# Kernel optimization log

Hardware: AMD Instinct MI355X
Metric: run time of the kernel (lower is better)

## Reference

```python
import jax, jax.numpy as jnp
import numpy as np

TEMPERATURE = 8.0  # sqrt(d_k) with d_k = 64


def setup_inputs() -> dict:
    key = jax.random.key(0)
    ks = jax.random.split(key, 5)
    shape = (64, 1024, 64)  # [B*H, N, d_k]
    return {
        "q": jax.random.normal(ks[0], shape, dtype=jnp.float32),
        "k": jax.random.normal(ks[1], shape, dtype=jnp.float32),
        "v": jax.random.normal(ks[2], shape, dtype=jnp.float32),
        "q_sem": jax.random.normal(ks[3], shape, dtype=jnp.float32),
        "k_sem": jax.random.normal(ks[4], shape, dtype=jnp.float32),
    }


def reference(q, k, v, q_sem, k_sem):
    # Semantic fusion branch (q_sem is not None): scores are recomputed
    # with the fused queries/keys. (The original also computes an unused
    # softmax over the pre-fusion scores and an unused attn_sem bmm --
    # dead code with no effect on outputs, so omitted.)
    qf = q + q_sem
    kf = k + k_sem
    attn_score = jnp.einsum("bnd,bmd->bnm", qf, kf) / TEMPERATURE  # [BH, N, N]
    attn = jax.nn.softmax(attn_score, axis=2)
    # dropout in eval mode == identity
    output = jnp.einsum("bnm,bmd->bnd", attn, v)  # [BH, N, d_k]
    return (output, attn, attn_score)
```

## Files before the change

kernel.cpp:

```cpp
#include <hip/hip_runtime.h>
#include <math.h>


#define BH 64
#define N 1024
#define D 64
#define TM 32
#define TK 128
#define NC (N / TK)
#define PSTR 1032
#define VSTR 136

typedef float    f32x4 __attribute__((ext_vector_type(4)));
typedef _Float16 half8 __attribute__((ext_vector_type(8)));
typedef _Float16 half4 __attribute__((ext_vector_type(4)));

__global__ __launch_bounds__(512, 2) void attn_mfma_kernel(
    const float* __restrict__ q, const float* __restrict__ k,
    const float* __restrict__ v, const float* __restrict__ qs,
    const float* __restrict__ ks,
    float* __restrict__ out_o, float* __restrict__ out_a,
    float* __restrict__ out_s)
{
    __shared__ __align__(16) _Float16 Pl[TM][PSTR];
    __shared__ __align__(16) _Float16 VT[2][D][VSTR];
    __shared__ float rsum[TM];

    const int t  = threadIdx.x;
    const int w  = t >> 6;
    const int l  = t & 63;
    const int lr = l & 15;
    const int lg = l >> 4;

    const int wg = blockIdx.x;
    const int b  = ((wg >> 8) << 3) | (wg & 7);
    const int q0 = ((wg >> 3) & 31) * TM;

    const size_t inb = (size_t)b * (N * D);
    const size_t sb  = (size_t)b * N * N + (size_t)q0 * N;

    if (t < TM) rsum[t] = 0.0f;

    half8 qa[2][2];
    {
        const float* qp  = q  + inb + (size_t)(q0 + lr) * D + lg * 8;
        const float* qsp = qs + inb + (size_t)(q0 + lr) * D + lg * 8;
#pragma unroll
        for (int mi = 0; mi < 2; ++mi) {
#pragma unroll
            for (int kst = 0; kst < 2; ++kst) {
                const float* p1 = qp  + mi * 16 * D + kst * 32;
                const float* p2 = qsp + mi * 16 * D + kst * 32;
                f32x4 a0 = *(const f32x4*)p1;
                f32x4 a1 = *(const f32x4*)(p1 + 4);
                f32x4 c0 = *(const f32x4*)p2;
                f32x4 c1 = *(const f32x4*)(p2 + 4);
                half8 h;
#pragma unroll
                for (int i = 0; i < 4; ++i) {
                    h[i]     = (_Float16)(a0[i] + c0[i]);
                    h[i + 4] = (_Float16)(a1[i] + c1[i]);
                }
                qa[mi][kst] = h;
            }
        }
    }
    __syncthreads();

    float rs[8];
#pragma unroll
    for (int i = 0; i < 8; ++i) rs[i] = 0.0f;

    const float* kp0 = k  + inb + (size_t)(w * 16 + lr) * D + lg * 8;
    const float* sp0 = ks + inb + (size_t)(w * 16 + lr) * D + lg * 8;

    f32x4 bufA[8], bufB[8];

    auto LD = [&](f32x4* bf, int kc) {
        const float* kp = kp0 + (size_t)kc * (TK * D);
        const float* sp = sp0 + (size_t)kc * (TK * D);
#pragma unroll
        for (int kst = 0; kst < 2; ++kst) {
            bf[kst * 2 + 0] = *(const f32x4*)(kp + kst * 32);
            bf[kst * 2 + 1] = *(const f32x4*)(kp + kst * 32 + 4);
            bf[kst * 2 + 4] = *(const f32x4*)(sp + kst * 32);
            bf[kst * 2 + 5] = *(const f32x4*)(sp + kst * 32 + 4);
        }
    };

    auto CHUNK = [&](const f32x4* bf, int kc) {
        half8 kb[2];
#pragma unroll
        for (int kst = 0; kst < 2; ++kst) {
            half8 h;
#pragma unroll
            for (int i = 0; i < 4; ++i) {
                h[i]     = (_Float16)(bf[kst * 2 + 0][i] + bf[kst * 2 + 4][i]);
                h[i + 4] = (_Float16)(bf[kst * 2 + 1][i] + bf[kst * 2 + 5][i]);
            }
            kb[kst] = h;
        }
        f32x4 ac0 = {0.f, 0.f, 0.f, 0.f}, ac1 = {0.f, 0.f, 0.f, 0.f};
        ac0 = __builtin_amdgcn_mfma_f32_16x16x32_f16(qa[0][0], kb[0], ac0, 0, 0, 0);
        ac0 = __builtin_amdgcn_mfma_f32_16x16x32_f16(qa[0][1], kb[1], ac0, 0, 0, 0);
        ac1 = __builtin_amdgcn_mfma_f32_16x16x32_f16(qa[1][0], kb[0], ac1, 0, 0, 0);
        ac1 = __builtin_amdgcn_mfma_f32_16x16x32_f16(qa[1][1], kb[1], ac1, 0, 0, 0);

        const int col = kc * TK + w * 16 + lr;
#pragma unroll
        for (int mi = 0; mi < 2; ++mi) {
            const f32x4 av = mi ? ac1 : ac0;
#pragma unroll
            for (int r = 0; r < 4; ++r) {
                const int row = mi * 16 + lg * 4 + r;
                const float sv = av[r] * 0.125f;
                __builtin_nontemporal_store(sv, out_s + sb + (size_t)row * N + col);
                const float pe = __expf(sv - 12.0f);
                rs[mi * 4 + r] += pe;
                Pl[row][col] = (_Float16)pe;
            }
        }
    };

    LD(bufA, 0);
#pragma unroll
    for (int kc = 0; kc < NC; ++kc) {
        const f32x4* cur = (kc & 1) ? bufB : bufA;
        f32x4* nxt = (kc & 1) ? bufA : bufB;
        if (kc + 1 < NC) LD(nxt, kc + 1);
        CHUNK(cur, kc);
    }

#pragma unroll
    for (int i = 0; i < 8; ++i) {
        float x = rs[i];
        x += __shfl_xor(x, 1);
        x += __shfl_xor(x, 2);
        x += __shfl_xor(x, 4);
        x += __shfl_xor(x, 8);
        rs[i] = x;
    }
    if (lr == 0) {
#pragma unroll
        for (int i = 0; i < 8; ++i) {
            const int row = (i >> 2) * 16 + lg * 4 + (i & 3);
            atomicAdd(&rsum[row], rs[i]);
        }
    }
    __syncthreads();

    const int mi2 = w >> 2, ni = w & 3;
    const int br4 = (t >> 4) * 4;
    const int bc4 = (t & 15) * 4;
    const int p3row = t >> 4;
    const int p3c = (t & 15) * 8;
    const float inv3 = 1.0f / rsum[p3row];

    f32x4 oc = {0.f, 0.f, 0.f, 0.f};

    auto VLOAD = [&](f32x4* vr, int kc) {
        const float* vp = v + inb + (size_t)(kc * TK + br4) * D + bc4;
#pragma unroll
        for (int j = 0; j < 4; ++j)
            vr[j] = *(const f32x4*)(vp + j * D);
    };
    auto VSTORE = [&](const f32x4* vr, int bs) {
#pragma unroll
        for (int c = 0; c < 4; ++c) {
            half4 hv = { (_Float16)vr[0][c], (_Float16)vr[1][c],
                         (_Float16)vr[2][c], (_Float16)vr[3][c] };
            *(half4*)&VT[bs][bc4 + c][br4] = hv;
        }
    };

    f32x4 vr[4];
    VLOAD(vr, 0);
    VSTORE(vr, 0);
    __syncthreads();

#pragma unroll
    for (int kc = 0; kc < NC; ++kc) {
        if (kc + 1 < NC) VLOAD(vr, kc + 1);

        {
            half8 ph = *(const half8*)&Pl[p3row][kc * TK + p3c];
            f32x4 a0, a1;
#pragma unroll
            for (int i = 0; i < 4; ++i) {
                a0[i] = (float)ph[i] * inv3;
                a1[i] = (float)ph[i + 4] * inv3;
            }
            float* ap = out_a + sb + (size_t)p3row * N + kc * TK + p3c;
            __builtin_nontemporal_store(a0, (f32x4*)ap);
            __builtin_nontemporal_store(a1, (f32x4*)(ap + 4));
        }

#pragma unroll
        for (int kst = 0; kst < 4; ++kst) {
            half8 pa = *(const half8*)&Pl[mi2 * 16 + lr][kc * TK + kst * 32 + lg * 8];
            half8 vb = *(const half8*)&VT[kc & 1][ni * 16 + lr][kst * 32 + lg * 8];
            oc = __builtin_amdgcn_mfma_f32_16x16x32_f16(pa, vb, oc, 0, 0, 0);
        }

        if (kc + 1 < NC) VSTORE(vr, (kc + 1) & 1);
        __syncthreads();
    }

#pragma unroll
    for (int r = 0; r < 4; ++r) {
        const int row = mi2 * 16 + lg * 4 + r;
        const float ov = oc[r] * (1.0f / rsum[row]);
        __builtin_nontemporal_store(ov, out_o + inb + (size_t)(q0 + row) * D + ni * 16 + lr);
    }
}

extern "C" void kernel_launch(void* const* d_in, const int* in_sizes, int n_in,
                              void* d_out, int out_size, void* d_ws, size_t ws_size,
                              hipStream_t stream) {
    const float* q  = (const float*)d_in[0];
    const float* k  = (const float*)d_in[1];
    const float* v  = (const float*)d_in[2];
    const float* qs = (const float*)d_in[3];
    const float* ks = (const float*)d_in[4];

    float* out_o = (float*)d_out;
    float* out_a = out_o + (size_t)BH * N * D;
    float* out_s = out_a + (size_t)BH * N * N;

    dim3 grid(BH * (N / TM));
    dim3 block(512);
    attn_mfma_kernel<<<grid, block, 0, stream>>>(q, k, v, qs, ks, out_o, out_a, out_s);
}
```

Baseline: 813.0 us.

## Fuse QK and PV phases into one loop with swizzled LDS and higher occupancy

Merges the score/exp pass and the P·V accumulation into a single chunk loop, so V loads and transposes overlap with the K work. Padded LDS strides are replaced by an XOR swizzle, the V buffer is single-buffered, and rsum reuses VT storage, which shrinks LDS so that launch bounds can request 4 blocks per CU. The normalized attention write-out moves to a separate pass after the loop. In exchange there are two barriers per chunk, the unrolled K loop is gone, and 4 blocks per CU puts more register pressure on each thread.

```diff
diff --git a/kernel.cpp b/kernel.cpp
--- a/kernel.cpp
+++ b/kernel.cpp
@@ -8,23 +8,23 @@
 #define TM 32
 #define TK 128
 #define NC (N / TK)
-#define PSTR 1032
-#define VSTR 136
 
 typedef float    f32x4 __attribute__((ext_vector_type(4)));
 typedef _Float16 half8 __attribute__((ext_vector_type(8)));
 typedef _Float16 half4 __attribute__((ext_vector_type(4)));
 
-__global__ __launch_bounds__(512, 2) void attn_mfma_kernel(
+__device__ __forceinline__ int swz(int row, int col) { return col ^ ((row & 7) << 3); }
+
+__global__ __launch_bounds__(512, 4) void attn_mfma_kernel(
     const float* __restrict__ q, const float* __restrict__ k,
     const float* __restrict__ v, const float* __restrict__ qs,
     const float* __restrict__ ks,
     float* __restrict__ out_o, float* __restrict__ out_a,
     float* __restrict__ out_s)
 {
-    __shared__ __align__(16) _Float16 Pl[TM][PSTR];
-    __shared__ __align__(16) _Float16 VT[2][D][VSTR];
-    __shared__ float rsum[TM];
+    __shared__ __align__(16) _Float16 Pl[TM][N];
+    __shared__ __align__(16) _Float16 VT[D][TK];
+    float* rsumf = (float*)&VT[0][0];
 
     const int t  = threadIdx.x;
     const int w  = t >> 6;
@@ -39,67 +39,84 @@
     const size_t inb = (size_t)b * (N * D);
     const size_t sb  = (size_t)b * N * N + (size_t)q0 * N;
 
-    if (t < TM) rsum[t] = 0.0f;
-
     half8 qa[2][2];
     {
         const float* qp  = q  + inb + (size_t)(q0 + lr) * D + lg * 8;
         const float* qsp = qs + inb + (size_t)(q0 + lr) * D + lg * 8;
 #pragma unroll
-        for (int mi = 0; mi < 2; ++mi) {
-#pragma unroll
-            for (int kst = 0; kst < 2; ++kst) {
-                const float* p1 = qp  + mi * 16 * D + kst * 32;
-                const float* p2 = qsp + mi * 16 * D + kst * 32;
-                f32x4 a0 = *(const f32x4*)p1;
-                f32x4 a1 = *(const f32x4*)(p1 + 4);
-                f32x4 c0 = *(const f32x4*)p2;
-                f32x4 c1 = *(const f32x4*)(p2 + 4);
-                half8 h;
-#pragma unroll
-                for (int i = 0; i < 4; ++i) {
-                    h[i]     = (_Float16)(a0[i] + c0[i]);
-                    h[i + 4] = (_Float16)(a1[i] + c1[i]);
-                }
-                qa[mi][kst] = h;
+        for (int mi = 0; mi < 2; ++mi)
+#pragma unroll
+        for (int kst = 0; kst < 2; ++kst) {
+            const float* p1 = qp  + mi * 16 * D + kst * 32;
+            const float* p2 = qsp + mi * 16 * D + kst * 32;
+            f32x4 a0 = *(const f32x4*)p1, a1 = *(const f32x4*)(p1 + 4);
+            f32x4 c0 = *(const f32x4*)p2, c1 = *(const f32x4*)(p2 + 4);
+            half8 h;
+#pragma unroll
+            for (int i = 0; i < 4; ++i) {
+                h[i]     = (_Float16)(a0[i] + c0[i]);
+                h[i + 4] = (_Float16)(a1[i] + c1[i]);
             }
-        }
-    }
-    __syncthreads();
-
-    float rs[8];
-#pragma unroll
-    for (int i = 0; i < 8; ++i) rs[i] = 0.0f;
+            qa[mi][kst] = h;
+        }
+    }
 
     const float* kp0 = k  + inb + (size_t)(w * 16 + lr) * D + lg * 8;
     const float* sp0 = ks + inb + (size_t)(w * 16 + lr) * D + lg * 8;
-
-    f32x4 bufA[8], bufB[8];
-
-    auto LD = [&](f32x4* bf, int kc) {
+    const int br4 = (t >> 4) * 4;
+    const int bc4 = (t & 15) * 4;
+
+    f32x4 kbuf[8];
+    f32x4 vr[4];
+
+    auto KLD = [&](int kc) {
         const float* kp = kp0 + (size_t)kc * (TK * D);
         const float* sp = sp0 + (size_t)kc * (TK * D);
-#pragma unroll
-        for (int kst = 0; kst < 2; ++kst) {
-            bf[kst * 2 + 0] = *(const f32x4*)(kp + kst * 32);
-            bf[kst * 2 + 1] = *(const f32x4*)(kp + kst * 32 + 4);
-            bf[kst * 2 + 4] = *(const f32x4*)(sp + kst * 32);
-            bf[kst * 2 + 5] = *(const f32x4*)(sp + kst * 32 + 4);
-        }
+        kbuf[0] = *(const f32x4*)(kp);
+        kbuf[1] = *(const f32x4*)(kp + 4);
+        kbuf[2] = *(const f32x4*)(kp + 32);
+        kbuf[3] = *(const f32x4*)(kp + 36);
+        kbuf[4] = *(const f32x4*)(sp);
+        kbuf[5] = *(const f32x4*)(sp + 4);
+        kbuf[6] = *(const f32x4*)(sp + 32);
+        kbuf[7] = *(const f32x4*)(sp + 36);
     };
-
-    auto CHUNK = [&](const f32x4* bf, int kc) {
+    auto VLOAD = [&](int kc) {
+        const float* vp = v + inb + (size_t)(kc * TK + br4) * D + bc4;
+#pragma unroll
+        for (int j = 0; j < 4; ++j) vr[j] = *(const f32x4*)(vp + j * D);
+    };
+
+    KLD(0);
+    VLOAD(0);
+
+    const int mi2 = w >> 2, ni = w & 3;
+    f32x4 oc = {0.f, 0.f, 0.f, 0.f};
+    float rs[8];
+#pragma unroll
+    for (int i = 0; i < 8; ++i) rs[i] = 0.f;
+
+    for (int kc = 0; kc < NC; ++kc) {
         half8 kb[2];
 #pragma unroll
         for (int kst = 0; kst < 2; ++kst) {
             half8 h;
 #pragma unroll
             for (int i = 0; i < 4; ++i) {
-                h[i]     = (_Float16)(bf[kst * 2 + 0][i] + bf[kst * 2 + 4][i]);
-                h[i + 4] = (_Float16)(bf[kst * 2 + 1][i] + bf[kst * 2 + 5][i]);
+                h[i]     = (_Float16)(kbuf[kst * 2][i]     + kbuf[kst * 2 + 4][i]);
+                h[i + 4] = (_Float16)(kbuf[kst * 2 + 1][i] + kbuf[kst * 2 + 5][i]);
             }
             kb[kst] = h;
         }
+#pragma unroll
+        for (int c = 0; c < 4; ++c) {
+            const int d = bc4 + c;
+            half4 hv = { (_Float16)vr[0][c], (_Float16)vr[1][c],
+                         (_Float16)vr[2][c], (_Float16)vr[3][c] };
+            *(half4*)&VT[d][swz(d, br4)] = hv;
+        }
+        if (kc + 1 < NC) { KLD(kc + 1); VLOAD(kc + 1); }
+
         f32x4 ac0 = {0.f, 0.f, 0.f, 0.f}, ac1 = {0.f, 0.f, 0.f, 0.f};
         ac0 = __builtin_amdgcn_mfma_f32_16x16x32_f16(qa[0][0], kb[0], ac0, 0, 0, 0);
         ac0 = __builtin_amdgcn_mfma_f32_16x16x32_f16(qa[0][1], kb[1], ac0, 0, 0, 0);
@@ -117,20 +134,23 @@
                 __builtin_nontemporal_store(sv, out_s + sb + (size_t)row * N + col);
                 const float pe = __expf(sv - 12.0f);
                 rs[mi * 4 + r] += pe;
-                Pl[row][col] = (_Float16)pe;
+                Pl[row][swz(row, col)] = (_Float16)pe;
             }
         }
-    };
-
-    LD(bufA, 0);
-#pragma unroll
-    for (int kc = 0; kc < NC; ++kc) {
-        const f32x4* cur = (kc & 1) ? bufB : bufA;
-        f32x4* nxt = (kc & 1) ? bufA : bufB;
-        if (kc + 1 < NC) LD(nxt, kc + 1);
-        CHUNK(cur, kc);
-    }
-
+        __syncthreads();
+
+#pragma unroll
+        for (int kst = 0; kst < 4; ++kst) {
+            const int ca = kc * TK + kst * 32 + lg * 8;
+            half8 pa = *(const half8*)&Pl[mi2 * 16 + lr][swz(mi2 * 16 + lr, ca)];
+            half8 vb = *(const half8*)&VT[ni * 16 + lr][swz(ni * 16 + lr, kst * 32 + lg * 8)];
+            oc = __builtin_amdgcn_mfma_f32_16x16x32_f16(pa, vb, oc, 0, 0, 0);
+        }
+        __syncthreads();
+    }
+
+    if (t < TM) rsumf[t] = 0.f;
+    __syncthreads();
 #pragma unroll
     for (int i = 0; i < 8; ++i) {
         float x = rs[i];
@@ -142,75 +162,33 @@
     }
     if (lr == 0) {
 #pragma unroll
-        for (int i = 0; i < 8; ++i) {
-            const int row = (i >> 2) * 16 + lg * 4 + (i & 3);
-            atomicAdd(&rsum[row], rs[i]);
-        }
+        for (int i = 0; i < 8; ++i)
+            atomicAdd(&rsumf[(i >> 2) * 16 + lg * 4 + (i & 3)], rs[i]);
     }
     __syncthreads();
-
-    const int mi2 = w >> 2, ni = w & 3;
-    const int br4 = (t >> 4) * 4;
-    const int bc4 = (t & 15) * 4;
-    const int p3row = t >> 4;
-    const int p3c = (t & 15) * 8;
-    const float inv3 = 1.0f / rsum[p3row];
-
-    f32x4 oc = {0.f, 0.f, 0.f, 0.f};
-
-    auto VLOAD = [&](f32x4* vr, int kc) {
-        const float* vp = v + inb + (size_t)(kc * TK + br4) * D + bc4;
-#pragma unroll
-        for (int j = 0; j < 4; ++j)
-            vr[j] = *(const f32x4*)(vp + j * D);
-    };
-    auto VSTORE = [&](const f32x4* vr, int bs) {
-#pragma unroll
-        for (int c = 0; c < 4; ++c) {
-            half4 hv = { (_Float16)vr[0][c], (_Float16)vr[1][c],
-                         (_Float16)vr[2][c], (_Float16)vr[3][c] };
-            *(half4*)&VT[bs][bc4 + c][br4] = hv;
-        }
-    };
-
-    f32x4 vr[4];
-    VLOAD(vr, 0);
-    VSTORE(vr, 0);
-    __syncthreads();
-
-#pragma unroll
-    for (int kc = 0; kc < NC; ++kc) {
-        if (kc + 1 < NC) VLOAD(vr, kc + 1);
-
-        {
-            half8 ph = *(const half8*)&Pl[p3row][kc * TK + p3c];
-            f32x4 a0, a1;
-#pragma unroll
-            for (int i = 0; i < 4; ++i) {
-                a0[i] = (float)ph[i] * inv3;
-                a1[i] = (float)ph[i + 4] * inv3;
-            }
-            float* ap = out_a + sb + (size_t)p3row * N + kc * TK + p3c;
-            __builtin_nontemporal_store(a0, (f32x4*)ap);
-            __builtin_nontemporal_store(a1, (f32x4*)(ap + 4));
-        }
-
-#pragma unroll
-        for (int kst = 0; kst < 4; ++kst) {
-            half8 pa = *(const half8*)&Pl[mi2 * 16 + lr][kc * TK + kst * 32 + lg * 8];
-            half8 vb = *(const half8*)&VT[kc & 1][ni * 16 + lr][kst * 32 + lg * 8];
-            oc = __builtin_amdgcn_mfma_f32_16x16x32_f16(pa, vb, oc, 0, 0, 0);
-        }
-
-        if (kc + 1 < NC) VSTORE(vr, (kc + 1) & 1);
-        __syncthreads();
-    }
 
 #pragma unroll
     for (int r = 0; r < 4; ++r) {
         const int row = mi2 * 16 + lg * 4 + r;
-        const float ov = oc[r] * (1.0f / rsum[row]);
+        const float ov = oc[r] * (1.0f / rsumf[row]);
         __builtin_nontemporal_store(ov, out_o + inb + (size_t)(q0 + row) * D + ni * 16 + lr);
+    }
+
+    const int p3row = t >> 4;
+    const int p3c   = (t & 15) * 8;
+    const float inv3 = 1.0f / rsumf[p3row];
+#pragma unroll
+    for (int cb = 0; cb < NC; ++cb) {
+        half8 ph = *(const half8*)&Pl[p3row][swz(p3row, cb * TK + p3c)];
+        f32x4 a0, a1;
+#pragma unroll
+        for (int i = 0; i < 4; ++i) {
+            a0[i] = (float)ph[i] * inv3;
+            a1[i] = (float)ph[i + 4] * inv3;
+        }
+        float* ap = out_a + sb + (size_t)p3row * N + cb * TK + p3c;
+        __builtin_nontemporal_store(a0, (f32x4*)ap);
+        __builtin_nontemporal_store(a1, (f32x4*)(ap + 4));
     }
 }
 
```

Measured after the change: 870.0 us. +7.0%, slower.
